# Kernel tuning notes

Measured on AMD Instinct MI355X. Metric: run time of the kernel, lower is better.

The kernel has to match this reference:

```python
import jax, jax.numpy as jnp
import numpy as np

N, M, NNZ = 100000, 20000, 1000000
IN_C, OUT_C, HEADS, FH = 128, 128, 4, 32  # FH = hidden_channels // heads
NEG_SLOPE = 0.2


def setup_inputs() -> dict:
    key = jax.random.key(0)
    ks = jax.random.split(key, 10)
    def glorot(k, shape):
        fan_in, fan_out = shape[-1], shape[-2] if len(shape) > 1 else shape[-1]
        s = jnp.sqrt(6.0 / (fan_in + fan_out))
        return jax.random.uniform(k, shape, jnp.float32, -s, s)
    return {
        "x": jax.random.normal(ks[0], (N, IN_C), jnp.float32),
        "hyperedge_attr": jax.random.normal(ks[1], (M, IN_C), jnp.float32),
        "lin1_W": glorot(ks[2], (HEADS * FH, IN_C)),
        "he_lin1_W": glorot(ks[3], (HEADS * FH, IN_C)),
        "att1": glorot(ks[4], (1, HEADS, 2 * FH)),
        "bias1": jnp.zeros((HEADS * FH,), jnp.float32),
        "lin2_W": glorot(ks[5], (OUT_C, HEADS * FH)),
        "bias2": jnp.zeros((OUT_C,), jnp.float32),
        "node_idx": jax.random.randint(ks[6], (NNZ,), 0, N),
        "edge_idx": jax.random.randint(ks[7], (NNZ,), 0, M),
    }


def _seg_softmax(logits, seg, num_seg):
    # segment-wise softmax over entries grouped by seg (PyG softmax)
    m = jax.ops.segment_max(logits, seg, num_segments=num_seg)
    m = jnp.where(jnp.isfinite(m), m, 0.0)  # empty segments
    e = jnp.exp(logits - m[seg])
    s = jax.ops.segment_sum(e, seg, num_segments=num_seg)
    return e / (s[seg] + 1e-16)


def reference(x, hyperedge_attr, lin1_W, he_lin1_W, att1, bias1, lin2_W, bias2,
              node_idx, edge_idx):
    n, m, nnz = x.shape[0], hyperedge_attr.shape[0], node_idx.shape[0]
    ones = jnp.ones((nnz,), x.dtype)
    deg = jax.ops.segment_sum(ones, node_idx, num_segments=n)      # D
    Dinv = jnp.where(deg > 0, 1.0 / deg, 0.0)
    bsz = jax.ops.segment_sum(ones, edge_idx, num_segments=m)      # B
    Binv = jnp.where(bsz > 0, 1.0 / bsz, 0.0)

    # ---- layer 1: attention conv, heads=4, concat ----
    x1 = (x @ lin1_W.T).reshape(n, HEADS, FH)                      # [N,H,F]
    he = (hyperedge_attr @ he_lin1_W.T).reshape(m, HEADS, FH)      # [M,H,F]
    a_i = (x1[node_idx] * att1[:, :, :FH]).sum(-1)                 # [nnz,H]
    a_j = (he[edge_idx] * att1[:, :, FH:]).sum(-1)
    alpha = jax.nn.leaky_relu(a_i + a_j, NEG_SLOPE)
    alpha = _seg_softmax(alpha, node_idx, n)                        # softmax per node

    # node -> hyperedge: B[e] * alpha * x1[node]
    msg = Binv[edge_idx][:, None, None] * x1[node_idx] * alpha[:, :, None]
    out_e = jax.ops.segment_sum(msg, edge_idx, num_segments=m)      # [M,H,F]
    # hyperedge -> node: D[v] * alpha * out_e[edge]
    msg = Dinv[node_idx][:, None, None] * out_e[edge_idx] * alpha[:, :, None]
    out_n = jax.ops.segment_sum(msg, node_idx, num_segments=n)      # [N,H,F]
    h = jax.nn.elu(out_n.reshape(n, HEADS * FH) + bias1)            # HCHA applies elu

    # ---- layer 2: plain conv (heads=1) ----
    x2 = h @ lin2_W.T                                               # [N,OUT_C]
    oe = jax.ops.segment_sum(Binv[edge_idx][:, None] * x2[node_idx],
                             edge_idx, num_segments=m)
    out = jax.ops.segment_sum(Dinv[node_idx][:, None] * oe[edge_idx],
                              node_idx, num_segments=n)
    return out + bias2
```

## Files before the change

### kernel.cpp

```cpp
#include <hip/hip_runtime.h>
#include <cstdint>


#define E_SHIFT 6
#define N_SHIFT 7
#define EB_CAP 4096
#define NB_CAP 2048
#define PCHUNK 4096
#define NBE_CAP 320
#define NBN_CAP 800

__device__ __forceinline__ unsigned wave_incl_scan(unsigned x) {
#pragma unroll
  for (int s = 1; s < 64; s <<= 1) {
    unsigned t = __shfl_up(x, s, 64);
    if ((int)(threadIdx.x & 63) >= s) x += t;
  }
  return x;
}

__global__ __launch_bounds__(256) void bucket_count(const int* __restrict__ node_idx,
                                                    const int* __restrict__ edge_idx,
                                                    unsigned* __restrict__ bcnt_e,
                                                    unsigned* __restrict__ bcnt_n, int nnz) {
  __shared__ unsigned he[NBE_CAP];
  __shared__ unsigned hn[NBN_CAP];
  const int t = threadIdx.x;
  const int base = blockIdx.x * PCHUNK;
  const int cnt = min(PCHUNK, nnz - base);
  for (int b = t; b < NBE_CAP; b += 256) he[b] = 0;
  for (int b = t; b < NBN_CAP; b += 256) hn[b] = 0;
  __syncthreads();
  for (int idx = t; idx < cnt; idx += 256) {
    unsigned e = (unsigned)edge_idx[base + idx];
    unsigned n = (unsigned)node_idx[base + idx];
    atomicAdd(&he[e >> E_SHIFT], 1u);
    atomicAdd(&hn[n >> N_SHIFT], 1u);
  }
  __syncthreads();
  for (int b = t; b < NBE_CAP; b += 256) if (he[b]) atomicAdd(&bcnt_e[b], he[b]);
  for (int b = t; b < NBN_CAP; b += 256) if (hn[b]) atomicAdd(&bcnt_n[b], hn[b]);
}

__global__ __launch_bounds__(1024) void bucket_scan(const unsigned* __restrict__ bcnt_e,
                                                    const unsigned* __restrict__ bcnt_n,
                                                    unsigned* __restrict__ bbase_e,
                                                    unsigned* __restrict__ bcur_e,
                                                    unsigned* __restrict__ bbase_n,
                                                    unsigned* __restrict__ bcur_n,
                                                    unsigned* __restrict__ eoff,
                                                    unsigned* __restrict__ noff,
                                                    int nbe, int nbn, int M_, int N_, int nnz) {
  __shared__ unsigned wsum[16];
  const int i = threadIdx.x;
  const int lane = i & 63, wid = i >> 6;
  {
    unsigned v = (i < nbe) ? bcnt_e[i] : 0u;
    unsigned incl = wave_incl_scan(v);
    if (lane == 63) wsum[wid] = incl;
    __syncthreads();
    unsigned add = 0;
    for (int w = 0; w < wid; ++w) add += wsum[w];
    unsigned excl = add + incl - v;
    if (i <= nbe) bbase_e[i] = excl;
    if (i < nbe) bcur_e[i] = excl;
    __syncthreads();
  }
  {
    unsigned v = (i < nbn) ? bcnt_n[i] : 0u;
    unsigned incl = wave_incl_scan(v);
    if (lane == 63) wsum[wid] = incl;
    __syncthreads();
    unsigned add = 0;
    for (int w = 0; w < wid; ++w) add += wsum[w];
    unsigned excl = add + incl - v;
    if (i <= nbn) bbase_n[i] = excl;
    if (i < nbn) bcur_n[i] = excl;
  }
  if (i == 0) { eoff[M_] = (unsigned)nnz; noff[N_] = (unsigned)nnz; }
}

__global__ __launch_bounds__(256) void partition2(const int* __restrict__ node_idx,
                                                  const int* __restrict__ edge_idx,
                                                  unsigned* __restrict__ bcur_e,
                                                  unsigned* __restrict__ bcur_n,
                                                  unsigned* __restrict__ tmp_e,
                                                  unsigned* __restrict__ tmp_n, int nnz) {
  __shared__ unsigned he[NBE_CAP];
  __shared__ unsigned hn[NBN_CAP];
  const int t = threadIdx.x;
  const int base = blockIdx.x * PCHUNK;
  const int cnt = min(PCHUNK, nnz - base);

  for (int b = t; b < NBE_CAP; b += 256) he[b] = 0;
  for (int b = t; b < NBN_CAP; b += 256) hn[b] = 0;
  __syncthreads();

  for (int idx = t; idx < cnt; idx += 256) {
    unsigned e = (unsigned)edge_idx[base + idx];
    unsigned n = (unsigned)node_idx[base + idx];
    atomicAdd(&he[e >> E_SHIFT], 1u);
    atomicAdd(&hn[n >> N_SHIFT], 1u);
  }
  __syncthreads();

  for (int b = t; b < NBE_CAP; b += 256) {
    unsigned c = he[b];
    he[b] = c ? atomicAdd(&bcur_e[b], c) : 0u;
  }
  for (int b = t; b < NBN_CAP; b += 256) {
    unsigned c = hn[b];
    hn[b] = c ? atomicAdd(&bcur_n[b], c) : 0u;
  }
  __syncthreads();

  for (int idx = t; idx < cnt; idx += 256) {
    unsigned e = (unsigned)edge_idx[base + idx];
    unsigned n = (unsigned)node_idx[base + idx];
    unsigned pe = atomicAdd(&he[e >> E_SHIFT], 1u);
    tmp_e[pe] = ((e & 63u) << 17) | n;
    unsigned pn = atomicAdd(&hn[n >> N_SHIFT], 1u);
    tmp_n[pn] = ((n & 127u) << 15) | e;
  }
}

__device__ __forceinline__ float4 alpha4(const float* __restrict__ ai,
                                         const float* __restrict__ aj,
                                         unsigned n, unsigned e) {
  float4 av = *(const float4*)&ai[(size_t)n * 4];
  float4 bv = *(const float4*)&aj[(size_t)e * 4];
  float v0 = av.x + bv.x, v1 = av.y + bv.y, v2 = av.z + bv.z, v3 = av.w + bv.w;
  v0 = v0 > 0.f ? v0 : 0.2f * v0;
  v1 = v1 > 0.f ? v1 : 0.2f * v1;
  v2 = v2 > 0.f ? v2 : 0.2f * v2;
  v3 = v3 > 0.f ? v3 : 0.2f * v3;
  return make_float4(expf(v0), expf(v1), expf(v2), expf(v3));
}

__global__ __launch_bounds__(256) void sort_node_exp(const unsigned* __restrict__ tmp,
                                                     const unsigned* __restrict__ bbase,
                                                     int N_,
                                                     const float* __restrict__ ai,
                                                     const float* __restrict__ aj,
                                                     float* __restrict__ ealpha_n,
                                                     int* __restrict__ neid,
                                                     unsigned* __restrict__ noff,
                                                     float* __restrict__ dinv) {
  __shared__ unsigned cur[128];
  __shared__ unsigned sbuf[NB_CAP];
  __shared__ unsigned wtot;
  int b = blockIdx.x, t = threadIdx.x;
  int n0 = b << N_SHIFT;
  unsigned base = bbase[b];
  int cnt = (int)(bbase[b + 1] - base);
  if (t < 128) cur[t] = 0;
  __syncthreads();
  for (int idx = t; idx < cnt; idx += 256) {
    unsigned key = tmp[base + idx] >> 15;
    atomicAdd(&cur[key], 1u);
  }
  __syncthreads();
  {
    unsigned c = (t < 128) ? cur[t] : 0u;
    unsigned incl = wave_incl_scan(c);
    if (t == 63) wtot = incl;
    __syncthreads();
    unsigned excl = incl - c + ((t >= 64 && t < 128) ? wtot : 0u);
    if (t < 128) {
      int n = n0 + t;
      if (n < N_) {
        noff[n] = base + excl;
        dinv[n] = c ? 1.f / (float)c : 0.f;
      }
      cur[t] = excl;
    }
  }
  __syncthreads();
  for (int idx = t; idx < cnt; idx += 256) {
    unsigned p = tmp[base + idx];
    unsigned key = p >> 15;
    unsigned pos = atomicAdd(&cur[key], 1u);
    if (pos < NB_CAP) {
      sbuf[pos] = p;
    } else {
      unsigned e = p & 0x7FFFu;
      *(float4*)&ealpha_n[(size_t)(base + pos) * 4] = alpha4(ai, aj, n0 + key, e);
      neid[base + pos] = (int)e;
    }
  }
  __syncthreads();
  int lim = min(cnt, NB_CAP);
  for (int idx = t; idx < lim; idx += 256) {
    unsigned p = sbuf[idx];
    unsigned key = p >> 15, e = p & 0x7FFFu;
    *(float4*)&ealpha_n[(size_t)(base + idx) * 4] = alpha4(ai, aj, n0 + key, e);
    neid[base + idx] = (int)e;
  }
}

__global__ __launch_bounds__(256) void node_denom2(const unsigned* __restrict__ noff,
                                                   const float* __restrict__ ealpha_n,
                                                   float* __restrict__ rden, int N) {
  int v = blockIdx.x * 256 + threadIdx.x;
  if (v >= N) return;
  unsigned s = noff[v], en = noff[v + 1];
  float x = 0.f, y = 0.f, z = 0.f, w = 0.f;
  for (unsigned j = s; j < en; ++j) {
    float4 a = *(const float4*)&ealpha_n[(size_t)j * 4];
    x += a.x; y += a.y; z += a.z; w += a.w;
  }
  *(float4*)&rden[(size_t)v * 4] = make_float4(1.f / (x + 1e-16f), 1.f / (y + 1e-16f),
                                               1.f / (z + 1e-16f), 1.f / (w + 1e-16f));
}

__global__ __launch_bounds__(256) void sort_edge_exp(const unsigned* __restrict__ tmp,
                                                     const unsigned* __restrict__ bbase,
                                                     int M_,
                                                     const float* __restrict__ ai,
                                                     const float* __restrict__ aj,
                                                     const float* __restrict__ rden,
                                                     float* __restrict__ alpha_e,
                                                     int* __restrict__ enid,
                                                     unsigned* __restrict__ eoff,
                                                     float* __restrict__ binv) {
  __shared__ unsigned cur[64];
  __shared__ float binv_s[64];
  __shared__ unsigned sbuf[EB_CAP];
  int b = blockIdx.x, t = threadIdx.x;
  int e0 = b << E_SHIFT;
  unsigned base = bbase[b];
  int cnt = (int)(bbase[b + 1] - base);
  if (t < 64) cur[t] = 0;
  __syncthreads();
  for (int idx = t; idx < cnt; idx += 256) {
    unsigned key = tmp[base + idx] >> 17;
    atomicAdd(&cur[key], 1u);
  }
  __syncthreads();
  {
    unsigned c = (t < 64) ? cur[t] : 0u;
    unsigned incl = wave_incl_scan(c);
    unsigned excl = incl - c;
    if (t < 64) {
      float bv = c ? 1.f / (float)c : 0.f;
      binv_s[t] = bv;
      int e = e0 + t;
      if (e < M_) {
        eoff[e] = base + excl;
        binv[e] = bv;
      }
      cur[t] = excl;
    }
  }
  __syncthreads();
  for (int idx = t; idx < cnt; idx += 256) {
    unsigned p = tmp[base + idx];
    unsigned key = p >> 17;
    unsigned pos = atomicAdd(&cur[key], 1u);
    if (pos < EB_CAP) {
      sbuf[pos] = p;
    } else {
      unsigned n = p & 0x1FFFFu;
      float4 al = alpha4(ai, aj, n, e0 + key);
      float4 rd = *(const float4*)&rden[(size_t)n * 4];
      float bv = binv_s[key];
      *(float4*)&alpha_e[(size_t)(base + pos) * 4] =
          make_float4(al.x * rd.x * bv, al.y * rd.y * bv, al.z * rd.z * bv, al.w * rd.w * bv);
      enid[base + pos] = (int)n;
    }
  }
  __syncthreads();
  int lim = min(cnt, EB_CAP);
  for (int idx = t; idx < lim; idx += 256) {
    unsigned p = sbuf[idx];
    unsigned key = p >> 17, n = p & 0x1FFFFu;
    float4 al = alpha4(ai, aj, n, e0 + key);
    float4 rd = *(const float4*)&rden[(size_t)n * 4];
    float bv = binv_s[key];
    *(float4*)&alpha_e[(size_t)(base + idx) * 4] =
        make_float4(al.x * rd.x * bv, al.y * rd.y * bv, al.z * rd.z * bv, al.w * rd.w * bv);
    enid[base + idx] = (int)n;
  }
}

__global__ __launch_bounds__(256) void wtrans(const float* __restrict__ W,
                                              float* __restrict__ WT) {
  int idx = blockIdx.x * 256 + threadIdx.x;
  if (idx >= 128 * 128) return;
  int k = idx >> 7, o = idx & 127;
  WT[idx] = W[o * 128 + k];
}

#define GM 64
__global__ __launch_bounds__(256) void gemm128t(const float* __restrict__ A,
                                                const float* __restrict__ WT,
                                                float* __restrict__ C, int rows,
                                                const float* __restrict__ att,
                                                float* __restrict__ aiout) {
  __shared__ __align__(16) float Ast[GM][132];
  const int tid = threadIdx.x;
  const int row0 = blockIdx.x * GM;

  for (int idx = tid; idx < GM * 32; idx += 256) {
    int r = idx >> 5, kq = idx & 31;
    int gr = row0 + r;
    float4 v = (gr < rows) ? *(const float4*)&A[(size_t)gr * 128 + kq * 4]
                           : make_float4(0.f, 0.f, 0.f, 0.f);
    *(float4*)&Ast[r][kq * 4] = v;
  }
  __syncthreads();

  const int tr = tid >> 5, tc = tid & 31;
  const int r0 = tr * 8, c0 = tc * 4;
  float acc[8][4] = {{0.f}};

  for (int k = 0; k < 128; k += 4) {
    float4 b0 = *(const float4*)&WT[(k + 0) * 128 + c0];
    float4 b1 = *(const float4*)&WT[(k + 1) * 128 + c0];
    float4 b2 = *(const float4*)&WT[(k + 2) * 128 + c0];
    float4 b3 = *(const float4*)&WT[(k + 3) * 128 + c0];
#pragma unroll
    for (int i = 0; i < 8; ++i) {
      float4 a = *(const float4*)&Ast[r0 + i][k];
      acc[i][0] += a.x * b0.x; acc[i][1] += a.x * b0.y; acc[i][2] += a.x * b0.z; acc[i][3] += a.x * b0.w;
      acc[i][0] += a.y * b1.x; acc[i][1] += a.y * b1.y; acc[i][2] += a.y * b1.z; acc[i][3] += a.y * b1.w;
      acc[i][0] += a.z * b2.x; acc[i][1] += a.z * b2.y; acc[i][2] += a.z * b2.z; acc[i][3] += a.z * b2.w;
      acc[i][0] += a.w * b3.x; acc[i][1] += a.w * b3.y; acc[i][2] += a.w * b3.z; acc[i][3] += a.w * b3.w;
    }
  }

#pragma unroll
  for (int i = 0; i < 8; ++i) {
    int gr = row0 + r0 + i;
    if (gr < rows)
      *(float4*)&C[(size_t)gr * 128 + c0] = make_float4(acc[i][0], acc[i][1], acc[i][2], acc[i][3]);
  }

  if (att) {
    int h = tc >> 3;
    float4 w = *(const float4*)&att[h * 64 + (c0 & 31)];
#pragma unroll
    for (int i = 0; i < 8; ++i) {
      float p = acc[i][0] * w.x + acc[i][1] * w.y + acc[i][2] * w.z + acc[i][3] * w.w;
      p += __shfl_xor(p, 1);
      p += __shfl_xor(p, 2);
      p += __shfl_xor(p, 4);
      if ((tc & 7) == 0) {
        int gr = row0 + r0 + i;
        if (gr < rows) aiout[(size_t)gr * 4 + h] = p;
      }
    }
  }
}

__global__ __launch_bounds__(256) void make_u(const float* __restrict__ W_he,
                                              const float* __restrict__ att1,
                                              float* __restrict__ u) {
  int idx = blockIdx.x * 256 + threadIdx.x;
  if (idx >= 512) return;
  int h = idx >> 7, k = idx & 127;
  float s = 0.f;
#pragma unroll
  for (int f = 0; f < 32; ++f)
    s += att1[h * 64 + 32 + f] * W_he[(size_t)(h * 32 + f) * 128 + k];
  u[h * 128 + k] = s;
}

__global__ __launch_bounds__(256) void att_dot_full(const float* __restrict__ feat,
                                                    const float* __restrict__ u,
                                                    float* __restrict__ outv, int rows) {
  int idx = blockIdx.x * 256 + threadIdx.x;
  if (idx >= rows * 4) return;
  int v = idx >> 2, h = idx & 3;
  const float4* fp = (const float4*)(feat + (size_t)v * 128);
  const float4* up = (const float4*)(u + h * 128);
  float s = 0.f;
#pragma unroll
  for (int q = 0; q < 32; ++q) {
    float4 a = up[q], f = fp[q];
    s += a.x * f.x + a.y * f.y + a.z * f.z + a.w * f.w;
  }
  outv[idx] = s;
}

__global__ __launch_bounds__(128) void edge_aggregate1(const float* __restrict__ x1,
                                                       const float* __restrict__ alpha_e,
                                                       const int* __restrict__ enid,
                                                       const unsigned* __restrict__ eoff,
                                                       float* __restrict__ out_e) {
  __shared__ float red[4][128];
  const int e = blockIdx.x, t = threadIdx.x;
  const int q = t >> 5, l = t & 31, hh = l >> 3;
  const unsigned s = eoff[e], en = eoff[e + 1];
  float4 A0 = make_float4(0.f, 0.f, 0.f, 0.f), A1 = A0, A2 = A0, A3 = A0;
  unsigned j = s + q;
  for (; j + 12 < en; j += 16) {
    int n0 = enid[j], n1 = enid[j + 4], n2 = enid[j + 8], n3 = enid[j + 12];
    float w0 = alpha_e[(size_t)j * 4 + hh];
    float w1 = alpha_e[(size_t)(j + 4) * 4 + hh];
    float w2 = alpha_e[(size_t)(j + 8) * 4 + hh];
    float w3 = alpha_e[(size_t)(j + 12) * 4 + hh];
    float4 a0 = *(const float4*)&x1[(size_t)n0 * 128 + l * 4];
    float4 a1 = *(const float4*)&x1[(size_t)n1 * 128 + l * 4];
    float4 a2 = *(const float4*)&x1[(size_t)n2 * 128 + l * 4];
    float4 a3 = *(const float4*)&x1[(size_t)n3 * 128 + l * 4];
    A0.x += w0 * a0.x; A0.y += w0 * a0.y; A0.z += w0 * a0.z; A0.w += w0 * a0.w;
    A1.x += w1 * a1.x; A1.y += w1 * a1.y; A1.z += w1 * a1.z; A1.w += w1 * a1.w;
    A2.x += w2 * a2.x; A2.y += w2 * a2.y; A2.z += w2 * a2.z; A2.w += w2 * a2.w;
    A3.x += w3 * a3.x; A3.y += w3 * a3.y; A3.z += w3 * a3.z; A3.w += w3 * a3.w;
  }
  for (; j < en; j += 4) {
    int n = enid[j];
    float w = alpha_e[(size_t)j * 4 + hh];
    float4 a = *(const float4*)&x1[(size_t)n * 128 + l * 4];
    A0.x += w * a.x; A0.y += w * a.y; A0.z += w * a.z; A0.w += w * a.w;
  }
  float4 A = make_float4((A0.x + A1.x) + (A2.x + A3.x), (A0.y + A1.y) + (A2.y + A3.y),
                         (A0.z + A1.z) + (A2.z + A3.z), (A0.w + A1.w) + (A2.w + A3.w));
  *(float4*)&red[q][l * 4] = A;
  __syncthreads();
  out_e[(size_t)e * 128 + t] = red[0][t] + red[1][t] + red[2][t] + red[3][t];
}

__global__ __launch_bounds__(128) void node_aggregate1(const float* __restrict__ out_e,
                                                       const float* __restrict__ ealpha_n,
                                                       const float* __restrict__ rden,
                                                       const float* __restrict__ dinv,
                                                       const float* __restrict__ bias1,
                                                       const int* __restrict__ neid,
                                                       const unsigned* __restrict__ noff,
                                                       float* __restrict__ hout) {
  __shared__ float red[4][128];
  const int v = blockIdx.x, t = threadIdx.x;
  const int q = t >> 5, l = t & 31, hh = l >> 3;
  const unsigned s = noff[v], en = noff[v + 1];
  float4 A0 = make_float4(0.f, 0.f, 0.f, 0.f), A1 = A0;
  unsigned j = s + q;
  for (; j + 4 < en; j += 8) {
    int e0 = neid[j], e1 = neid[j + 4];
    float w0 = ealpha_n[(size_t)j * 4 + hh];
    float w1 = ealpha_n[(size_t)(j + 4) * 4 + hh];
    float4 a0 = *(const float4*)&out_e[(size_t)e0 * 128 + l * 4];
    float4 a1 = *(const float4*)&out_e[(size_t)e1 * 128 + l * 4];
    A0.x += w0 * a0.x; A0.y += w0 * a0.y; A0.z += w0 * a0.z; A0.w += w0 * a0.w;
    A1.x += w1 * a1.x; A1.y += w1 * a1.y; A1.z += w1 * a1.z; A1.w += w1 * a1.w;
  }
  for (; j < en; j += 4) {
    int e0 = neid[j];
    float w = ealpha_n[(size_t)j * 4 + hh];
    float4 a = *(const float4*)&out_e[(size_t)e0 * 128 + l * 4];
    A0.x += w * a.x; A0.y += w * a.y; A0.z += w * a.z; A0.w += w * a.w;
  }
  float4 A = make_float4(A0.x + A1.x, A0.y + A1.y, A0.z + A1.z, A0.w + A1.w);
  *(float4*)&red[q][l * 4] = A;
  __syncthreads();
  float rd = dinv[v] * rden[(size_t)v * 4 + (t >> 5)];
  float val = rd * (red[0][t] + red[1][t] + red[2][t] + red[3][t]) + bias1[t];
  hout[(size_t)v * 128 + t] = val > 0.f ? val : expm1f(val);
}

__global__ __launch_bounds__(128) void edge_aggregate2(const float* __restrict__ hfeat,
                                                       const float* __restrict__ binv,
                                                       const int* __restrict__ enid,
                                                       const unsigned* __restrict__ eoff,
                                                       float* __restrict__ oe) {
  __shared__ float red[4][128];
  const int e = blockIdx.x, t = threadIdx.x;
  const int q = t >> 5, l = t & 31;
  const unsigned s = eoff[e], en = eoff[e + 1];
  float4 A0 = make_float4(0.f, 0.f, 0.f, 0.f), A1 = A0, A2 = A0, A3 = A0;
  unsigned j = s + q;
  for (; j + 12 < en; j += 16) {
    int n0 = enid[j], n1 = enid[j + 4], n2 = enid[j + 8], n3 = enid[j + 12];
    float4 a0 = *(const float4*)&hfeat[(size_t)n0 * 128 + l * 4];
    float4 a1 = *(const float4*)&hfeat[(size_t)n1 * 128 + l * 4];
    float4 a2 = *(const float4*)&hfeat[(size_t)n2 * 128 + l * 4];
    float4 a3 = *(const float4*)&hfeat[(size_t)n3 * 128 + l * 4];
    A0.x += a0.x; A0.y += a0.y; A0.z += a0.z; A0.w += a0.w;
    A1.x += a1.x; A1.y += a1.y; A1.z += a1.z; A1.w += a1.w;
    A2.x += a2.x; A2.y += a2.y; A2.z += a2.z; A2.w += a2.w;
    A3.x += a3.x; A3.y += a3.y; A3.z += a3.z; A3.w += a3.w;
  }
  for (; j < en; j += 4) {
    int n = enid[j];
    float4 a = *(const float4*)&hfeat[(size_t)n * 128 + l * 4];
    A0.x += a.x; A0.y += a.y; A0.z += a.z; A0.w += a.w;
  }
  float4 A = make_float4((A0.x + A1.x) + (A2.x + A3.x), (A0.y + A1.y) + (A2.y + A3.y),
                         (A0.z + A1.z) + (A2.z + A3.z), (A0.w + A1.w) + (A2.w + A3.w));
  *(float4*)&red[q][l * 4] = A;
  __syncthreads();
  oe[(size_t)e * 128 + t] = binv[e] * (red[0][t] + red[1][t] + red[2][t] + red[3][t]);
}

__global__ __launch_bounds__(128) void node_aggregate2(const float* __restrict__ oe2,
                                                       const float* __restrict__ dinv,
                                                       const float* __restrict__ bias2,
                                                       const int* __restrict__ neid,
                                                       const unsigned* __restrict__ noff,
                                                       float* __restrict__ out) {
  __shared__ float red[4][128];
  const int v = blockIdx.x, t = threadIdx.x;
  const int q = t >> 5, l = t & 31;
  const unsigned s = noff[v], en = noff[v + 1];
  float4 A0 = make_float4(0.f, 0.f, 0.f, 0.f), A1 = A0;
  unsigned j = s + q;
  for (; j + 4 < en; j += 8) {
    int e0 = neid[j], e1 = neid[j + 4];
    float4 a0 = *(const float4*)&oe2[(size_t)e0 * 128 + l * 4];
    float4 a1 = *(const float4*)&oe2[(size_t)e1 * 128 + l * 4];
    A0.x += a0.x; A0.y += a0.y; A0.z += a0.z; A0.w += a0.w;
    A1.x += a1.x; A1.y += a1.y; A1.z += a1.z; A1.w += a1.w;
  }
  for (; j < en; j += 4) {
    int e0 = neid[j];
    float4 a = *(const float4*)&oe2[(size_t)e0 * 128 + l * 4];
    A0.x += a.x; A0.y += a.y; A0.z += a.z; A0.w += a.w;
  }
  float4 A = make_float4(A0.x + A1.x, A0.y + A1.y, A0.z + A1.z, A0.w + A1.w);
  *(float4*)&red[q][l * 4] = A;
  __syncthreads();
  out[(size_t)v * 128 + t] = dinv[v] * (red[0][t] + red[1][t] + red[2][t] + red[3][t]) + bias2[t];
}

extern "C" void kernel_launch(void* const* d_in, const int* in_sizes, int n_in,
                              void* d_out, int out_size, void* d_ws, size_t ws_size,
                              hipStream_t stream) {
  (void)n_in; (void)out_size; (void)ws_size;
  const float* x      = (const float*)d_in[0];
  const float* hea    = (const float*)d_in[1];
  const float* lin1W  = (const float*)d_in[2];
  const float* helinW = (const float*)d_in[3];
  const float* att1   = (const float*)d_in[4];
  const float* bias1  = (const float*)d_in[5];
  const float* lin2W  = (const float*)d_in[6];
  const float* bias2  = (const float*)d_in[7];
  const int* node_idx = (const int*)d_in[8];
  const int* edge_idx = (const int*)d_in[9];
  float* out = (float*)d_out;

  const int N   = in_sizes[0] / 128;
  const int M   = in_sizes[1] / 128;
  const int NNZ = in_sizes[8];
  const int NBE = (M + 63) >> E_SHIFT;
  const int NBN = (N + 127) >> N_SHIFT;

  char* base = (char*)d_ws;
  size_t off = 0;
  auto alloc = [&](size_t bytes) -> char* {
    char* p = base + off;
    off = (off + bytes + 255) & ~(size_t)255;
    return p;
  };
  float* x1    = (float*)alloc((size_t)N * 128 * 4);
  float* hbuf  = (float*)alloc((size_t)N * 128 * 4);
  float* heoe  = (float*)alloc((size_t)M * 128 * 4);
  float* ai    = (float*)alloc((size_t)N * 4 * 4);
  float* aj    = (float*)alloc((size_t)M * 4 * 4);
  float* u     = (float*)alloc(512 * 4);
  float* WT1   = (float*)alloc(128 * 128 * 4);
  float* WT2   = (float*)alloc(128 * 128 * 4);
  float* dinv  = (float*)alloc((size_t)N * 4);
  float* binv  = (float*)alloc((size_t)M * 4);
  float* rden  = (float*)alloc((size_t)N * 4 * 4);
  char* zstart = base + off;
  unsigned* bcnt_e = (unsigned*)alloc((size_t)NBE * 4);
  unsigned* bcnt_n = (unsigned*)alloc((size_t)NBN * 4);
  size_t zbytes = (size_t)((base + off) - zstart);
  float* alpha_e  = (float*)alloc((size_t)NNZ * 4 * 4);
  float* ealpha_n = (float*)alloc((size_t)NNZ * 4 * 4);
  unsigned* tmp_e = (unsigned*)alloc((size_t)NNZ * 4);
  unsigned* tmp_n = (unsigned*)alloc((size_t)NNZ * 4);
  unsigned* noff  = (unsigned*)alloc((size_t)(N + 1) * 4);
  unsigned* eoff  = (unsigned*)alloc((size_t)(M + 1) * 4);
  unsigned* bbase_e = (unsigned*)alloc((size_t)(NBE + 1) * 4);
  unsigned* bbase_n = (unsigned*)alloc((size_t)(NBN + 1) * 4);
  unsigned* bcur_e = (unsigned*)alloc((size_t)NBE * 4);
  unsigned* bcur_n = (unsigned*)alloc((size_t)NBN * 4);
  int* enid       = (int*)alloc((size_t)NNZ * 4);
  int* neid       = (int*)alloc((size_t)NNZ * 4);

  hipMemsetAsync(zstart, 0, zbytes, stream);

  const int g_pchunk = (NNZ + PCHUNK - 1) / PCHUNK;
  bucket_count<<<g_pchunk, 256, 0, stream>>>(node_idx, edge_idx, bcnt_e, bcnt_n, NNZ);
  bucket_scan<<<1, 1024, 0, stream>>>(bcnt_e, bcnt_n, bbase_e, bcur_e, bbase_n, bcur_n,
                                      eoff, noff, NBE, NBN, M, N, NNZ);
  partition2<<<g_pchunk, 256, 0, stream>>>(node_idx, edge_idx, bcur_e, bcur_n,
                                           tmp_e, tmp_n, NNZ);

  wtrans<<<64, 256, 0, stream>>>(lin1W, WT1);
  wtrans<<<64, 256, 0, stream>>>(lin2W, WT2);
  gemm128t<<<(N + GM - 1) / GM, 256, 0, stream>>>(x, WT1, x1, N, att1, ai);
  make_u<<<2, 256, 0, stream>>>(helinW, att1, u);
  att_dot_full<<<(M * 4 + 255) / 256, 256, 0, stream>>>(hea, u, aj, M);

  sort_node_exp<<<NBN, 256, 0, stream>>>(tmp_n, bbase_n, N, ai, aj, ealpha_n, neid,
                                         noff, dinv);
  node_denom2<<<(N + 255) / 256, 256, 0, stream>>>(noff, ealpha_n, rden, N);
  sort_edge_exp<<<NBE, 256, 0, stream>>>(tmp_e, bbase_e, M, ai, aj, rden, alpha_e, enid,
                                         eoff, binv);

  edge_aggregate1<<<M, 128, 0, stream>>>(x1, alpha_e, enid, eoff, heoe);
  node_aggregate1<<<N, 128, 0, stream>>>(heoe, ealpha_n, rden, dinv, bias1, neid, noff, hbuf);

  edge_aggregate2<<<M, 128, 0, stream>>>(hbuf, binv, enid, eoff, heoe);
  gemm128t<<<(M + GM - 1) / GM, 256, 0, stream>>>(heoe, WT2, x1, M, nullptr, nullptr);
  node_aggregate2<<<N, 128, 0, stream>>>(x1, dinv, bias2, neid, noff, out);
}
```

Before: 470.1 us.

## Sort buckets by secondary key and fuse softmax denominator into node sort

The per-bucket counting sort now keys on both the local segment id and the high bits of the other index, so entries within each node or hyperedge are grouped by neighbour range, which should give better gather locality in the later aggregation kernels. The node softmax denominator is accumulated with shared-memory float atomics inside sort_node_exp, and the separate node_denom2 kernel is removed. The cost is a larger shared histogram and a wider multi-wave scan per block, plus float atomic contention on the shared denominators. Floating-point summation order also becomes nondeterministic.

```diff
diff --git a/kernel.cpp b/kernel.cpp
--- a/kernel.cpp
+++ b/kernel.cpp
@@ -6,6 +6,8 @@
 #define N_SHIFT 7
 #define EB_CAP 4096
 #define NB_CAP 2048
+#define EKEYS 4096
+#define NKEYS 2048
 #define PCHUNK 4096
 #define NBE_CAP 320
 #define NBN_CAP 800
@@ -145,46 +147,63 @@
                                                      float* __restrict__ ealpha_n,
                                                      int* __restrict__ neid,
                                                      unsigned* __restrict__ noff,
-                                                     float* __restrict__ dinv) {
-  __shared__ unsigned cur[128];
+                                                     float* __restrict__ dinv,
+                                                     float* __restrict__ rden) {
+  __shared__ unsigned cur[NKEYS];
   __shared__ unsigned sbuf[NB_CAP];
-  __shared__ unsigned wtot;
+  __shared__ __align__(16) float dsum[128][4];
+  __shared__ unsigned wsum[4];
   int b = blockIdx.x, t = threadIdx.x;
   int n0 = b << N_SHIFT;
   unsigned base = bbase[b];
   int cnt = (int)(bbase[b + 1] - base);
-  if (t < 128) cur[t] = 0;
-  __syncthreads();
-  for (int idx = t; idx < cnt; idx += 256) {
-    unsigned key = tmp[base + idx] >> 15;
-    atomicAdd(&cur[key], 1u);
-  }
-  __syncthreads();
-  {
-    unsigned c = (t < 128) ? cur[t] : 0u;
-    unsigned incl = wave_incl_scan(c);
-    if (t == 63) wtot = incl;
-    __syncthreads();
-    unsigned excl = incl - c + ((t >= 64 && t < 128) ? wtot : 0u);
-    if (t < 128) {
-      int n = n0 + t;
-      if (n < N_) {
-        noff[n] = base + excl;
-        dinv[n] = c ? 1.f / (float)c : 0.f;
-      }
-      cur[t] = excl;
-    }
-  }
+  for (int i = t; i < NKEYS; i += 256) cur[i] = 0;
+  for (int i = t; i < 512; i += 256) ((float*)dsum)[i] = 0.f;
   __syncthreads();
   for (int idx = t; idx < cnt; idx += 256) {
     unsigned p = tmp[base + idx];
-    unsigned key = p >> 15;
+    unsigned key = ((p >> 15) << 4) | ((p & 0x7FFFu) >> 11);
+    atomicAdd(&cur[key], 1u);
+  }
+  __syncthreads();
+  {
+    unsigned loc[8]; unsigned tot = 0;
+#pragma unroll
+    for (int i = 0; i < 8; ++i) { loc[i] = cur[t * 8 + i]; tot += loc[i]; }
+    unsigned incl = wave_incl_scan(tot);
+    int lane = t & 63, wid = t >> 6;
+    if (lane == 63) wsum[wid] = incl;
+    __syncthreads();
+    unsigned add = 0;
+    for (int w = 0; w < wid; ++w) add += wsum[w];
+    unsigned run = add + incl - tot;
+#pragma unroll
+    for (int i = 0; i < 8; ++i) { cur[t * 8 + i] = run; run += loc[i]; }
+  }
+  __syncthreads();
+  if (t < 128) {
+    unsigned s0 = cur[t * 16];
+    unsigned s1 = (t == 127) ? (unsigned)cnt : cur[(t + 1) * 16];
+    unsigned c = s1 - s0;
+    int n = n0 + t;
+    if (n < N_) {
+      noff[n] = base + s0;
+      dinv[n] = c ? 1.f / (float)c : 0.f;
+    }
+  }
+  __syncthreads();
+  for (int idx = t; idx < cnt; idx += 256) {
+    unsigned p = tmp[base + idx];
+    unsigned key = ((p >> 15) << 4) | ((p & 0x7FFFu) >> 11);
     unsigned pos = atomicAdd(&cur[key], 1u);
     if (pos < NB_CAP) {
       sbuf[pos] = p;
     } else {
-      unsigned e = p & 0x7FFFu;
-      *(float4*)&ealpha_n[(size_t)(base + pos) * 4] = alpha4(ai, aj, n0 + key, e);
+      unsigned nl = p >> 15, e = p & 0x7FFFu;
+      float4 al = alpha4(ai, aj, n0 + nl, e);
+      atomicAdd(&dsum[nl][0], al.x); atomicAdd(&dsum[nl][1], al.y);
+      atomicAdd(&dsum[nl][2], al.z); atomicAdd(&dsum[nl][3], al.w);
+      *(float4*)&ealpha_n[(size_t)(base + pos) * 4] = al;
       neid[base + pos] = (int)e;
     }
   }
@@ -192,25 +211,22 @@
   int lim = min(cnt, NB_CAP);
   for (int idx = t; idx < lim; idx += 256) {
     unsigned p = sbuf[idx];
-    unsigned key = p >> 15, e = p & 0x7FFFu;
-    *(float4*)&ealpha_n[(size_t)(base + idx) * 4] = alpha4(ai, aj, n0 + key, e);
+    unsigned nl = p >> 15, e = p & 0x7FFFu;
+    float4 al = alpha4(ai, aj, n0 + nl, e);
+    atomicAdd(&dsum[nl][0], al.x); atomicAdd(&dsum[nl][1], al.y);
+    atomicAdd(&dsum[nl][2], al.z); atomicAdd(&dsum[nl][3], al.w);
+    *(float4*)&ealpha_n[(size_t)(base + idx) * 4] = al;
     neid[base + idx] = (int)e;
   }
-}
-
-__global__ __launch_bounds__(256) void node_denom2(const unsigned* __restrict__ noff,
-                                                   const float* __restrict__ ealpha_n,
-                                                   float* __restrict__ rden, int N) {
-  int v = blockIdx.x * 256 + threadIdx.x;
-  if (v >= N) return;
-  unsigned s = noff[v], en = noff[v + 1];
-  float x = 0.f, y = 0.f, z = 0.f, w = 0.f;
-  for (unsigned j = s; j < en; ++j) {
-    float4 a = *(const float4*)&ealpha_n[(size_t)j * 4];
-    x += a.x; y += a.y; z += a.z; w += a.w;
-  }
-  *(float4*)&rden[(size_t)v * 4] = make_float4(1.f / (x + 1e-16f), 1.f / (y + 1e-16f),
-                                               1.f / (z + 1e-16f), 1.f / (w + 1e-16f));
+  __syncthreads();
+  if (t < 128) {
+    int n = n0 + t;
+    if (n < N_) {
+      *(float4*)&rden[(size_t)n * 4] =
+          make_float4(1.f / (dsum[t][0] + 1e-16f), 1.f / (dsum[t][1] + 1e-16f),
+                      1.f / (dsum[t][2] + 1e-16f), 1.f / (dsum[t][3] + 1e-16f));
+    }
+  }
 }
 
 __global__ __launch_bounds__(256) void sort_edge_exp(const unsigned* __restrict__ tmp,
@@ -223,47 +239,61 @@
                                                      int* __restrict__ enid,
                                                      unsigned* __restrict__ eoff,
                                                      float* __restrict__ binv) {
-  __shared__ unsigned cur[64];
+  __shared__ unsigned cur[EKEYS];
+  __shared__ unsigned sbuf[EB_CAP];
   __shared__ float binv_s[64];
-  __shared__ unsigned sbuf[EB_CAP];
+  __shared__ unsigned wsum[4];
   int b = blockIdx.x, t = threadIdx.x;
   int e0 = b << E_SHIFT;
   unsigned base = bbase[b];
   int cnt = (int)(bbase[b + 1] - base);
-  if (t < 64) cur[t] = 0;
-  __syncthreads();
-  for (int idx = t; idx < cnt; idx += 256) {
-    unsigned key = tmp[base + idx] >> 17;
-    atomicAdd(&cur[key], 1u);
-  }
-  __syncthreads();
-  {
-    unsigned c = (t < 64) ? cur[t] : 0u;
-    unsigned incl = wave_incl_scan(c);
-    unsigned excl = incl - c;
-    if (t < 64) {
-      float bv = c ? 1.f / (float)c : 0.f;
-      binv_s[t] = bv;
-      int e = e0 + t;
-      if (e < M_) {
-        eoff[e] = base + excl;
-        binv[e] = bv;
-      }
-      cur[t] = excl;
-    }
-  }
+  for (int i = t; i < EKEYS; i += 256) cur[i] = 0;
   __syncthreads();
   for (int idx = t; idx < cnt; idx += 256) {
     unsigned p = tmp[base + idx];
-    unsigned key = p >> 17;
+    unsigned key = ((p >> 17) << 6) | ((p & 0x1FFFFu) >> 11);
+    atomicAdd(&cur[key], 1u);
+  }
+  __syncthreads();
+  {
+    unsigned loc[16]; unsigned tot = 0;
+#pragma unroll
+    for (int i = 0; i < 16; ++i) { loc[i] = cur[t * 16 + i]; tot += loc[i]; }
+    unsigned incl = wave_incl_scan(tot);
+    int lane = t & 63, wid = t >> 6;
+    if (lane == 63) wsum[wid] = incl;
+    __syncthreads();
+    unsigned add = 0;
+    for (int w = 0; w < wid; ++w) add += wsum[w];
+    unsigned run = add + incl - tot;
+#pragma unroll
+    for (int i = 0; i < 16; ++i) { cur[t * 16 + i] = run; run += loc[i]; }
+  }
+  __syncthreads();
+  if (t < 64) {
+    unsigned s0 = cur[t * 64];
+    unsigned s1 = (t == 63) ? (unsigned)cnt : cur[(t + 1) * 64];
+    unsigned c = s1 - s0;
+    float bv = c ? 1.f / (float)c : 0.f;
+    binv_s[t] = bv;
+    int e = e0 + t;
+    if (e < M_) {
+      eoff[e] = base + s0;
+      binv[e] = bv;
+    }
+  }
+  __syncthreads();
+  for (int idx = t; idx < cnt; idx += 256) {
+    unsigned p = tmp[base + idx];
+    unsigned key = ((p >> 17) << 6) | ((p & 0x1FFFFu) >> 11);
     unsigned pos = atomicAdd(&cur[key], 1u);
     if (pos < EB_CAP) {
       sbuf[pos] = p;
     } else {
-      unsigned n = p & 0x1FFFFu;
-      float4 al = alpha4(ai, aj, n, e0 + key);
+      unsigned n = p & 0x1FFFFu, el = p >> 17;
+      float4 al = alpha4(ai, aj, n, e0 + el);
       float4 rd = *(const float4*)&rden[(size_t)n * 4];
-      float bv = binv_s[key];
+      float bv = binv_s[el];
       *(float4*)&alpha_e[(size_t)(base + pos) * 4] =
           make_float4(al.x * rd.x * bv, al.y * rd.y * bv, al.z * rd.z * bv, al.w * rd.w * bv);
       enid[base + pos] = (int)n;
@@ -273,10 +303,10 @@
   int lim = min(cnt, EB_CAP);
   for (int idx = t; idx < lim; idx += 256) {
     unsigned p = sbuf[idx];
-    unsigned key = p >> 17, n = p & 0x1FFFFu;
-    float4 al = alpha4(ai, aj, n, e0 + key);
+    unsigned n = p & 0x1FFFFu, el = p >> 17;
+    float4 al = alpha4(ai, aj, n, e0 + el);
     float4 rd = *(const float4*)&rden[(size_t)n * 4];
-    float bv = binv_s[key];
+    float bv = binv_s[el];
     *(float4*)&alpha_e[(size_t)(base + idx) * 4] =
         make_float4(al.x * rd.x * bv, al.y * rd.y * bv, al.z * rd.z * bv, al.w * rd.w * bv);
     enid[base + idx] = (int)n;
@@ -596,8 +626,7 @@
   att_dot_full<<<(M * 4 + 255) / 256, 256, 0, stream>>>(hea, u, aj, M);
 
   sort_node_exp<<<NBN, 256, 0, stream>>>(tmp_n, bbase_n, N, ai, aj, ealpha_n, neid,
-                                         noff, dinv);
-  node_denom2<<<(N + 255) / 256, 256, 0, stream>>>(noff, ealpha_n, rden, N);
+                                         noff, dinv, rden);
   sort_edge_exp<<<NBE, 256, 0, stream>>>(tmp_e, bbase_e, M, ai, aj, rden, alpha_e, enid,
                                          eoff, binv);
 
```

Measured after the change: 491.1 us. +4.5%, slower.

## Precompute per-block partition cursors and fuse softmax denominators into node sort

Applied to the files above, without the earlier changes.

bucket_count now saves each block's histogram. A new cursor_scan kernel scans those histograms per bucket into exact write cursors, so partition2 no longer recounts its chunk or does global atomic cursor grabs. Separately, sort_node_exp builds the per-node exp sums with shared-memory float atomics and writes rden directly, which removes the node_denom2 kernel and its second pass over ealpha_n. The cost is two extra per-block histogram arrays, two more kernel launches with strided column reads in cursor_scan, and float atomics that make the summation order nondeterministic.

```diff
diff --git a/kernel.cpp b/kernel.cpp
--- a/kernel.cpp
+++ b/kernel.cpp
@@ -22,7 +22,9 @@
 __global__ __launch_bounds__(256) void bucket_count(const int* __restrict__ node_idx,
                                                     const int* __restrict__ edge_idx,
                                                     unsigned* __restrict__ bcnt_e,
-                                                    unsigned* __restrict__ bcnt_n, int nnz) {
+                                                    unsigned* __restrict__ bcnt_n,
+                                                    unsigned* __restrict__ pcnt_e,
+                                                    unsigned* __restrict__ pcnt_n, int nnz) {
   __shared__ unsigned he[NBE_CAP];
   __shared__ unsigned hn[NBN_CAP];
   const int t = threadIdx.x;
@@ -38,16 +40,20 @@
     atomicAdd(&hn[n >> N_SHIFT], 1u);
   }
   __syncthreads();
-  for (int b = t; b < NBE_CAP; b += 256) if (he[b]) atomicAdd(&bcnt_e[b], he[b]);
-  for (int b = t; b < NBN_CAP; b += 256) if (hn[b]) atomicAdd(&bcnt_n[b], hn[b]);
+  for (int b = t; b < NBE_CAP; b += 256) {
+    pcnt_e[(size_t)blockIdx.x * NBE_CAP + b] = he[b];
+    if (he[b]) atomicAdd(&bcnt_e[b], he[b]);
+  }
+  for (int b = t; b < NBN_CAP; b += 256) {
+    pcnt_n[(size_t)blockIdx.x * NBN_CAP + b] = hn[b];
+    if (hn[b]) atomicAdd(&bcnt_n[b], hn[b]);
+  }
 }
 
 __global__ __launch_bounds__(1024) void bucket_scan(const unsigned* __restrict__ bcnt_e,
                                                     const unsigned* __restrict__ bcnt_n,
                                                     unsigned* __restrict__ bbase_e,
-                                                    unsigned* __restrict__ bcur_e,
                                                     unsigned* __restrict__ bbase_n,
-                                                    unsigned* __restrict__ bcur_n,
                                                     unsigned* __restrict__ eoff,
                                                     unsigned* __restrict__ noff,
                                                     int nbe, int nbn, int M_, int N_, int nnz) {
@@ -63,7 +69,6 @@
     for (int w = 0; w < wid; ++w) add += wsum[w];
     unsigned excl = add + incl - v;
     if (i <= nbe) bbase_e[i] = excl;
-    if (i < nbe) bcur_e[i] = excl;
     __syncthreads();
   }
   {
@@ -75,15 +80,37 @@
     for (int w = 0; w < wid; ++w) add += wsum[w];
     unsigned excl = add + incl - v;
     if (i <= nbn) bbase_n[i] = excl;
-    if (i < nbn) bcur_n[i] = excl;
   }
   if (i == 0) { eoff[M_] = (unsigned)nnz; noff[N_] = (unsigned)nnz; }
+}
+
+__global__ __launch_bounds__(256) void cursor_scan(const unsigned* __restrict__ pcnt,
+                                                   const unsigned* __restrict__ bbase,
+                                                   unsigned* __restrict__ pcur,
+                                                   int nblocks, int cap) {
+  __shared__ unsigned wsum[4];
+  const int k = blockIdx.x, t = threadIdx.x;
+  const int lane = t & 63, wid = t >> 6;
+  unsigned carry = bbase[k];
+  for (int b0 = 0; b0 < nblocks; b0 += 256) {
+    int b = b0 + t;
+    unsigned v = (b < nblocks) ? pcnt[(size_t)b * cap + k] : 0u;
+    unsigned incl = wave_incl_scan(v);
+    if (lane == 63) wsum[wid] = incl;
+    __syncthreads();
+    unsigned add = 0;
+    for (int w = 0; w < wid; ++w) add += wsum[w];
+    if (b < nblocks) pcur[(size_t)b * cap + k] = carry + add + incl - v;
+    unsigned tot = wsum[0] + wsum[1] + wsum[2] + wsum[3];
+    __syncthreads();
+    carry += tot;
+  }
 }
 
 __global__ __launch_bounds__(256) void partition2(const int* __restrict__ node_idx,
                                                   const int* __restrict__ edge_idx,
-                                                  unsigned* __restrict__ bcur_e,
-                                                  unsigned* __restrict__ bcur_n,
+                                                  const unsigned* __restrict__ pcur_e,
+                                                  const unsigned* __restrict__ pcur_n,
                                                   unsigned* __restrict__ tmp_e,
                                                   unsigned* __restrict__ tmp_n, int nnz) {
   __shared__ unsigned he[NBE_CAP];
@@ -92,26 +119,8 @@
   const int base = blockIdx.x * PCHUNK;
   const int cnt = min(PCHUNK, nnz - base);
 
-  for (int b = t; b < NBE_CAP; b += 256) he[b] = 0;
-  for (int b = t; b < NBN_CAP; b += 256) hn[b] = 0;
-  __syncthreads();
-
-  for (int idx = t; idx < cnt; idx += 256) {
-    unsigned e = (unsigned)edge_idx[base + idx];
-    unsigned n = (unsigned)node_idx[base + idx];
-    atomicAdd(&he[e >> E_SHIFT], 1u);
-    atomicAdd(&hn[n >> N_SHIFT], 1u);
-  }
-  __syncthreads();
-
-  for (int b = t; b < NBE_CAP; b += 256) {
-    unsigned c = he[b];
-    he[b] = c ? atomicAdd(&bcur_e[b], c) : 0u;
-  }
-  for (int b = t; b < NBN_CAP; b += 256) {
-    unsigned c = hn[b];
-    hn[b] = c ? atomicAdd(&bcur_n[b], c) : 0u;
-  }
+  for (int b = t; b < NBE_CAP; b += 256) he[b] = pcur_e[(size_t)blockIdx.x * NBE_CAP + b];
+  for (int b = t; b < NBN_CAP; b += 256) hn[b] = pcur_n[(size_t)blockIdx.x * NBN_CAP + b];
   __syncthreads();
 
   for (int idx = t; idx < cnt; idx += 256) {
@@ -145,15 +154,18 @@
                                                      float* __restrict__ ealpha_n,
                                                      int* __restrict__ neid,
                                                      unsigned* __restrict__ noff,
-                                                     float* __restrict__ dinv) {
+                                                     float* __restrict__ dinv,
+                                                     float* __restrict__ rden) {
   __shared__ unsigned cur[128];
   __shared__ unsigned sbuf[NB_CAP];
+  __shared__ __align__(16) float dsum[128][4];
   __shared__ unsigned wtot;
   int b = blockIdx.x, t = threadIdx.x;
   int n0 = b << N_SHIFT;
   unsigned base = bbase[b];
   int cnt = (int)(bbase[b + 1] - base);
   if (t < 128) cur[t] = 0;
+  for (int i = t; i < 512; i += 256) ((float*)dsum)[i] = 0.f;
   __syncthreads();
   for (int idx = t; idx < cnt; idx += 256) {
     unsigned key = tmp[base + idx] >> 15;
@@ -184,7 +196,10 @@
       sbuf[pos] = p;
     } else {
       unsigned e = p & 0x7FFFu;
-      *(float4*)&ealpha_n[(size_t)(base + pos) * 4] = alpha4(ai, aj, n0 + key, e);
+      float4 al = alpha4(ai, aj, n0 + key, e);
+      atomicAdd(&dsum[key][0], al.x); atomicAdd(&dsum[key][1], al.y);
+      atomicAdd(&dsum[key][2], al.z); atomicAdd(&dsum[key][3], al.w);
+      *(float4*)&ealpha_n[(size_t)(base + pos) * 4] = al;
       neid[base + pos] = (int)e;
     }
   }
@@ -192,25 +207,22 @@
   int lim = min(cnt, NB_CAP);
   for (int idx = t; idx < lim; idx += 256) {
     unsigned p = sbuf[idx];
-    unsigned key = p >> 15, e = p & 0x7FFFu;
-    *(float4*)&ealpha_n[(size_t)(base + idx) * 4] = alpha4(ai, aj, n0 + key, e);
+    unsigned nl = p >> 15, e = p & 0x7FFFu;
+    float4 al = alpha4(ai, aj, n0 + nl, e);
+    atomicAdd(&dsum[nl][0], al.x); atomicAdd(&dsum[nl][1], al.y);
+    atomicAdd(&dsum[nl][2], al.z); atomicAdd(&dsum[nl][3], al.w);
+    *(float4*)&ealpha_n[(size_t)(base + idx) * 4] = al;
     neid[base + idx] = (int)e;
   }
-}
-
-__global__ __launch_bounds__(256) void node_denom2(const unsigned* __restrict__ noff,
-                                                   const float* __restrict__ ealpha_n,
-                                                   float* __restrict__ rden, int N) {
-  int v = blockIdx.x * 256 + threadIdx.x;
-  if (v >= N) return;
-  unsigned s = noff[v], en = noff[v + 1];
-  float x = 0.f, y = 0.f, z = 0.f, w = 0.f;
-  for (unsigned j = s; j < en; ++j) {
-    float4 a = *(const float4*)&ealpha_n[(size_t)j * 4];
-    x += a.x; y += a.y; z += a.z; w += a.w;
-  }
-  *(float4*)&rden[(size_t)v * 4] = make_float4(1.f / (x + 1e-16f), 1.f / (y + 1e-16f),
-                                               1.f / (z + 1e-16f), 1.f / (w + 1e-16f));
+  __syncthreads();
+  if (t < 128) {
+    int n = n0 + t;
+    if (n < N_) {
+      *(float4*)&rden[(size_t)n * 4] =
+          make_float4(1.f / (dsum[t][0] + 1e-16f), 1.f / (dsum[t][1] + 1e-16f),
+                      1.f / (dsum[t][2] + 1e-16f), 1.f / (dsum[t][3] + 1e-16f));
+    }
+  }
 }
 
 __global__ __launch_bounds__(256) void sort_edge_exp(const unsigned* __restrict__ tmp,
@@ -544,6 +556,7 @@
   const int NNZ = in_sizes[8];
   const int NBE = (M + 63) >> E_SHIFT;
   const int NBN = (N + 127) >> N_SHIFT;
+  const int g_pchunk = (NNZ + PCHUNK - 1) / PCHUNK;
 
   char* base = (char*)d_ws;
   size_t off = 0;
@@ -575,18 +588,22 @@
   unsigned* eoff  = (unsigned*)alloc((size_t)(M + 1) * 4);
   unsigned* bbase_e = (unsigned*)alloc((size_t)(NBE + 1) * 4);
   unsigned* bbase_n = (unsigned*)alloc((size_t)(NBN + 1) * 4);
-  unsigned* bcur_e = (unsigned*)alloc((size_t)NBE * 4);
-  unsigned* bcur_n = (unsigned*)alloc((size_t)NBN * 4);
+  unsigned* pcnt_e = (unsigned*)alloc((size_t)g_pchunk * NBE_CAP * 4);
+  unsigned* pcnt_n = (unsigned*)alloc((size_t)g_pchunk * NBN_CAP * 4);
+  unsigned* pcur_e = (unsigned*)alloc((size_t)g_pchunk * NBE_CAP * 4);
+  unsigned* pcur_n = (unsigned*)alloc((size_t)g_pchunk * NBN_CAP * 4);
   int* enid       = (int*)alloc((size_t)NNZ * 4);
   int* neid       = (int*)alloc((size_t)NNZ * 4);
 
   hipMemsetAsync(zstart, 0, zbytes, stream);
 
-  const int g_pchunk = (NNZ + PCHUNK - 1) / PCHUNK;
-  bucket_count<<<g_pchunk, 256, 0, stream>>>(node_idx, edge_idx, bcnt_e, bcnt_n, NNZ);
-  bucket_scan<<<1, 1024, 0, stream>>>(bcnt_e, bcnt_n, bbase_e, bcur_e, bbase_n, bcur_n,
+  bucket_count<<<g_pchunk, 256, 0, stream>>>(node_idx, edge_idx, bcnt_e, bcnt_n,
+                                             pcnt_e, pcnt_n, NNZ);
+  bucket_scan<<<1, 1024, 0, stream>>>(bcnt_e, bcnt_n, bbase_e, bbase_n,
                                       eoff, noff, NBE, NBN, M, N, NNZ);
-  partition2<<<g_pchunk, 256, 0, stream>>>(node_idx, edge_idx, bcur_e, bcur_n,
+  cursor_scan<<<NBE, 256, 0, stream>>>(pcnt_e, bbase_e, pcur_e, g_pchunk, NBE_CAP);
+  cursor_scan<<<NBN, 256, 0, stream>>>(pcnt_n, bbase_n, pcur_n, g_pchunk, NBN_CAP);
+  partition2<<<g_pchunk, 256, 0, stream>>>(node_idx, edge_idx, pcur_e, pcur_n,
                                            tmp_e, tmp_n, NNZ);
 
   wtrans<<<64, 256, 0, stream>>>(lin1W, WT1);
@@ -596,8 +613,7 @@
   att_dot_full<<<(M * 4 + 255) / 256, 256, 0, stream>>>(hea, u, aj, M);
 
   sort_node_exp<<<NBN, 256, 0, stream>>>(tmp_n, bbase_n, N, ai, aj, ealpha_n, neid,
-                                         noff, dinv);
-  node_denom2<<<(N + 255) / 256, 256, 0, stream>>>(noff, ealpha_n, rden, N);
+                                         noff, dinv, rden);
   sort_edge_exp<<<NBE, 256, 0, stream>>>(tmp_e, bbase_e, M, ai, aj, rden, alpha_e, enid,
                                          eoff, binv);
 
```

Measured after the change: 498.4 us. 6.0% more time.
